# Kernel tuning notes

Hardware: AMD Instinct MI355X
Metric: run time of the kernel (lower is better)

Reference implementation:

```python
import jax, jax.numpy as jnp
import numpy as np
from jax import lax

N_NODES = 4096
M_EDGES = 16384
PDHG_ITERS = 300
POWER_ITERS = 20


def setup_inputs() -> dict:
    key = jax.random.key(0)
    kA, kb, kc = jax.random.split(key, 3)
    A = jax.random.normal(kA, (N_NODES - 2, M_EDGES), dtype=jnp.float32)
    b = jax.random.uniform(kb, (M_EDGES,), dtype=jnp.float32)  # capacities >= 0
    c = jax.random.normal(kc, (M_EDGES,), dtype=jnp.float32)
    return {"A": A, "b": b, "c": c}


def _spectral_norm(A):
    # Power iteration on A^T A; gradients stopped (step sizes are hyperparams).
    A = lax.stop_gradient(A)
    v0 = jnp.ones((A.shape[1],), A.dtype)
    v0 = v0 / jnp.linalg.norm(v0)

    def body(i, v):
        w = A.T @ (A @ v)
        return w / jnp.linalg.norm(w)

    v = lax.fori_loop(0, POWER_ITERS, body, v0)
    return jnp.sqrt(jnp.linalg.norm(A.T @ (A @ v)))


def _solve_lp(A, b, c):
    # LP:  max -c^T x  s.t.  0 <= x <= b,  A x = 0
    # <=>  min  c^T x  s.t.  x in [0, b],  A x = 0
    # Solved with PDHG (Chambolle-Pock):
    #   x <- clip(x - tau*(c + A^T y), 0, b)
    #   y <- y + sigma * A (2 x_new - x_old)
    nrm = _spectral_norm(A)
    tau = 0.9 / nrm
    sigma = 0.9 / nrm

    x0 = jnp.zeros((A.shape[1],), A.dtype)  # x = 0 is always feasible
    y0 = jnp.zeros((A.shape[0],), A.dtype)

    def step(carry, _):
        x, y = carry
        x_new = jnp.clip(x - tau * (c + A.T @ y), 0.0, b)
        y_new = y + sigma * (A @ (2.0 * x_new - x))
        return (x_new, y_new), None

    (x, y), _ = lax.scan(step, (x0, y0), None, length=PDHG_ITERS)
    return x


def reference(A, b, c):
    solution = _solve_lp(A, b, c)
    # objective == 'cost': solution.mul(-c).sum()
    return jnp.sum(solution * (-c))
```

## Files before the change

### kernel.cpp

```cpp
#include <hip/hip_runtime.h>


constexpr int N_ROWS = 4094;
constexpr int NPAD   = 4096;
constexpr int M_COLS = 16384;
constexpr int M4     = M_COLS / 4;
constexpr int PDHG_ITERS  = 300;
constexpr int POWER_ITERS = 8;
constexpr int P_CHUNKS = 64;
constexpr int ROWS_PER_CHUNK = 64;
constexpr int FJ = 32;
constexpr int FBLOCKS = M_COLS / FJ;
constexpr int AZ_J  = 64;
constexpr int AZ_CH = M_COLS / AZ_J;

typedef _Float16 half8  __attribute__((ext_vector_type(8)));
typedef _Float16 half4v __attribute__((ext_vector_type(4)));
typedef _Float16 half2v __attribute__((ext_vector_type(2)));
typedef _Float16 half_t;
typedef float f32x2 __attribute__((ext_vector_type(2)));

__device__ __forceinline__ void dec8(uint2 w, float* f) {
    f32x2 a = __builtin_amdgcn_cvt_pk_f32_fp8(w.x, false);
    f32x2 b = __builtin_amdgcn_cvt_pk_f32_fp8(w.x, true);
    f32x2 c = __builtin_amdgcn_cvt_pk_f32_fp8(w.y, false);
    f32x2 d = __builtin_amdgcn_cvt_pk_f32_fp8(w.y, true);
    f[0]=a[0]; f[1]=a[1]; f[2]=b[0]; f[3]=b[1];
    f[4]=c[0]; f[5]=c[1]; f[6]=d[0]; f[7]=d[1];
}

__global__ __launch_bounds__(256) void k_init(float* __restrict__ x,
                                              float* __restrict__ v,
                                              float* __restrict__ y,
                                              float* __restrict__ t) {
    int j = blockIdx.x * 256 + threadIdx.x;
    if (j < M_COLS) { x[j] = 0.f; v[j] = 0.0078125f; }
    if (j < NPAD) { y[j] = 0.f; t[j] = 0.f; }
}

__global__ __launch_bounds__(256) void k_transpose_both(const float* __restrict__ A,
                                                        unsigned int* __restrict__ AT8,
                                                        half_t* __restrict__ AT16) {
    __shared__ float tile[64][65];
    const int i0 = blockIdx.x * 64;
    const int j0 = blockIdx.y * 64;
    const int t = threadIdx.x;
    const float4* __restrict__ A4 = reinterpret_cast<const float4*>(A);
#pragma unroll
    for (int k = 0; k < 4; ++k) {
        int idx = k * 256 + t;
        int r = idx >> 4, c4 = idx & 15;
        int i = i0 + r;
        float4 val = (i < N_ROWS) ? A4[(size_t)i * M4 + (j0 >> 2) + c4]
                                  : make_float4(0.f, 0.f, 0.f, 0.f);
        tile[r][c4 * 4 + 0] = val.x;
        tile[r][c4 * 4 + 1] = val.y;
        tile[r][c4 * 4 + 2] = val.z;
        tile[r][c4 * 4 + 3] = val.w;
    }
    __syncthreads();
    const int it_p = i0 >> 9;
    const int sub  = (i0 >> 8) & 1;
    const int l0   = (i0 & 255) >> 2;
#pragma unroll
    for (int k = 0; k < 4; ++k) {
        int idx = k * 256 + t;
        int j = idx >> 4, lofs = idx & 15;
        float f0 = tile[lofs * 4 + 0][j] * 64.f;
        float f1 = tile[lofs * 4 + 1][j] * 64.f;
        float f2 = tile[lofs * 4 + 2][j] * 64.f;
        float f3 = tile[lofs * 4 + 3][j] * 64.f;
        int r = 0;
        r = __builtin_amdgcn_cvt_pk_fp8_f32(f0, f1, r, false);
        r = __builtin_amdgcn_cvt_pk_fp8_f32(f2, f3, r, true);
        AT8[(size_t)(j0 + j) * 1024 + it_p * 128 + (l0 + lofs) * 2 + sub] = (unsigned int)r;
    }
    half8* __restrict__ O8 = reinterpret_cast<half8*>(AT16);
#pragma unroll
    for (int k = 0; k < 2; ++k) {
        int idx = k * 256 + t;
        int j = idx >> 3, q = idx & 7;
        half8 h;
#pragma unroll
        for (int e = 0; e < 8; ++e) h[e] = (half_t)tile[q * 8 + e][j];
        O8[((size_t)(j0 + j) * NPAD + i0) / 8 + q] = h;
    }
}

__global__ __launch_bounds__(256) void k_fused8(const unsigned int* __restrict__ AT,
                                                const float* __restrict__ y,
                                                const float* __restrict__ c,
                                                const float* __restrict__ b,
                                                float* __restrict__ x,
                                                half_t* __restrict__ partial,
                                                const float* __restrict__ scalars) {
    __shared__ float ybuf[4096];
    const int tid = threadIdx.x;
    const int wv = tid >> 6, lane = tid & 63;
    {
        const float4* __restrict__ y4 = reinterpret_cast<const float4*>(y);
        float4* s4 = reinterpret_cast<float4*>(ybuf);
#pragma unroll
        for (int k = 0; k < 4; ++k) s4[k * 256 + tid] = y4[k * 256 + tid];
    }
    __syncthreads();
    const float tau = scalars[1];
    const int j0 = blockIdx.x * FJ + wv * 8;
    const uint2* __restrict__ A2 = reinterpret_cast<const uint2*>(AT);

    float xs = 0.f, cs = 0.f, bs = 0.f, xkeep = 0.f;
    if (lane < 8) {
        xs = x[j0 + lane];
        cs = c[j0 + lane];
        bs = b[j0 + lane];
    }

    float acc[64];
#pragma unroll
    for (int q = 0; q < 64; ++q) acc[q] = 0.f;

    uint2 cur[8], nxt[8];
#pragma unroll
    for (int p = 0; p < 8; ++p) cur[p] = A2[(size_t)j0 * 512 + p * 64 + lane];

    for (int q = 0; q < 8; ++q) {
        const int j = j0 + q;
        if (q + 1 < 8) {
#pragma unroll
            for (int p = 0; p < 8; ++p) nxt[p] = A2[(size_t)(j + 1) * 512 + p * 64 + lane];
        }
        float s = 0.f;
#pragma unroll
        for (int p = 0; p < 8; ++p) {
            float f[8];
            dec8(cur[p], f);
            const float4 ya = *reinterpret_cast<const float4*>(&ybuf[p * 512 + lane * 4]);
            const float4 yb = *reinterpret_cast<const float4*>(&ybuf[p * 512 + 256 + lane * 4]);
            s = fmaf(f[0], ya.x, s);
            s = fmaf(f[1], ya.y, s);
            s = fmaf(f[2], ya.z, s);
            s = fmaf(f[3], ya.w, s);
            s = fmaf(f[4], yb.x, s);
            s = fmaf(f[5], yb.y, s);
            s = fmaf(f[6], yb.z, s);
            s = fmaf(f[7], yb.w, s);
        }
#pragma unroll
        for (int o = 1; o < 64; o <<= 1) s += __shfl_xor(s, o, 64);
        s *= 0.015625f;
        float xo = __shfl(xs, q, 64);
        float cj = __shfl(cs, q, 64);
        float bj = __shfl(bs, q, 64);
        float xn = xo - tau * (cj + s);
        xn = fminf(fmaxf(xn, 0.f), bj);
        if (lane == q) xkeep = xn;
        float z = 2.f * xn - xo;
#pragma unroll
        for (int p = 0; p < 8; ++p) {
            float f[8];
            dec8(cur[p], f);
#pragma unroll
            for (int e = 0; e < 8; ++e)
                acc[p * 8 + e] = fmaf(f[e], z, acc[p * 8 + e]);
        }
#pragma unroll
        for (int p = 0; p < 8; ++p) cur[p] = nxt[p];
    }
    if (lane < 8) x[j0 + lane] = xkeep;

    __syncthreads();
    for (int w = 0; w < 4; ++w) {
        if (wv == w) {
#pragma unroll
            for (int p = 0; p < 8; ++p) {
                float4* pa = reinterpret_cast<float4*>(&ybuf[p * 512 + lane * 4]);
                float4* pb = reinterpret_cast<float4*>(&ybuf[p * 512 + 256 + lane * 4]);
                float4 va = make_float4(acc[p * 8 + 0], acc[p * 8 + 1], acc[p * 8 + 2], acc[p * 8 + 3]);
                float4 vb = make_float4(acc[p * 8 + 4], acc[p * 8 + 5], acc[p * 8 + 6], acc[p * 8 + 7]);
                if (w == 0) { *pa = va; *pb = vb; }
                else {
                    float4 oa = *pa, ob = *pb;
                    oa.x += va.x; oa.y += va.y; oa.z += va.z; oa.w += va.w;
                    ob.x += vb.x; ob.y += vb.y; ob.z += vb.z; ob.w += vb.w;
                    *pa = oa; *pb = ob;
                }
            }
        }
        __syncthreads();
    }
    half_t* __restrict__ ph = partial + (size_t)blockIdx.x * 4096;
    const float4* __restrict__ S4 = reinterpret_cast<const float4*>(ybuf);
#pragma unroll
    for (int k = 0; k < 4; ++k) {
        float4 vv = S4[k * 256 + tid];
        half4v h;
        h[0] = (half_t)vv.x; h[1] = (half_t)vv.y; h[2] = (half_t)vv.z; h[3] = (half_t)vv.w;
        *reinterpret_cast<half4v*>(&ph[k * 1024 + tid * 4]) = h;
    }
}

template <int NP>
__global__ __launch_bounds__(256) void k_merge_h(const half_t* __restrict__ partial,
                                                 float* __restrict__ y,
                                                 const float* __restrict__ scalars) {
    __shared__ float2 smf[256];
    const int tid = threadIdx.x;
    const int mb = blockIdx.x;
    const int rp = tid & 7;
    const int kk = tid >> 3;
    const half2v* __restrict__ ph2 = reinterpret_cast<const half2v*>(partial);
    float sx = 0.f, sy = 0.f;
#pragma unroll
    for (int q = 0; q < NP / 32; ++q) {
        int p = kk * (NP / 32) + q;
        half2v h = ph2[(size_t)p * 2048 + mb * 8 + rp];
        sx += (float)h[0];
        sy += (float)h[1];
    }
    smf[kk * 8 + rp] = make_float2(sx, sy);
    __syncthreads();
    if (tid < 16) {
        int pairIdx = tid >> 1, comp = tid & 1;
        float tot = 0.f;
#pragma unroll
        for (int k2 = 0; k2 < 32; ++k2) {
            float2 f2 = smf[k2 * 8 + pairIdx];
            tot += comp ? f2.y : f2.x;
        }
        y[mb * 16 + tid] += scalars[2] * tot;
    }
}

template <int NP>
__global__ __launch_bounds__(256) void k_merge0(const float* __restrict__ partial,
                                                float* __restrict__ out) {
    constexpr int PER = NP / 16;
    const int tid = threadIdx.x;
    const int r = tid & 15, k = tid >> 4;
    const int row = blockIdx.x * 16 + r;
    const float* __restrict__ p0 = partial + (size_t)k * PER * NPAD + row;
    float s = 0.f;
#pragma unroll 8
    for (int q = 0; q < PER; ++q) s += p0[(size_t)q * NPAD];
    __shared__ float sm[256];
    sm[tid] = s;
    __syncthreads();
    if (tid < 16) {
        const int orow = blockIdx.x * 16 + tid;
        float tot = 0.f;
#pragma unroll
        for (int kk = 0; kk < 16; ++kk) tot += sm[kk * 16 + tid];
        out[orow] = tot;
    }
}

__global__ __launch_bounds__(256) void k_colp8(const unsigned int* __restrict__ AT,
                                               const float* __restrict__ u,
                                               float* __restrict__ w) {
    const int wv = threadIdx.x >> 6, lane = threadIdx.x & 63;
    const int j = blockIdx.x * 4 + wv;
    const uint2* __restrict__ A2 = reinterpret_cast<const uint2*>(AT);
    const float4* __restrict__ u4 = reinterpret_cast<const float4*>(u);
    float s = 0.f;
#pragma unroll
    for (int p = 0; p < 8; ++p) {
        float f[8];
        dec8(A2[(size_t)j * 512 + p * 64 + lane], f);
        float4 ua = u4[p * 128 + lane];
        float4 ub = u4[p * 128 + 64 + lane];
        s = fmaf(f[0], ua.x, s);
        s = fmaf(f[1], ua.y, s);
        s = fmaf(f[2], ua.z, s);
        s = fmaf(f[3], ua.w, s);
        s = fmaf(f[4], ub.x, s);
        s = fmaf(f[5], ub.y, s);
        s = fmaf(f[6], ub.z, s);
        s = fmaf(f[7], ub.w, s);
    }
#pragma unroll
    for (int o = 1; o < 64; o <<= 1) s += __shfl_xor(s, o, 64);
    if (lane == 0) w[j] = s;
}

__global__ __launch_bounds__(256) void k_azp8(const unsigned int* __restrict__ AT,
                                              const float* __restrict__ zv,
                                              float* __restrict__ partial) {
    const int ch = blockIdx.y;
    const int j0 = ch * AZ_J;
    const int p = blockIdx.x * 256 + threadIdx.x;
    __shared__ float sz[AZ_J];
    if (threadIdx.x < AZ_J) sz[threadIdx.x] = zv[j0 + threadIdx.x];
    __syncthreads();
    const uint2* __restrict__ A2 = reinterpret_cast<const uint2*>(AT);
    float acc[8];
#pragma unroll
    for (int e = 0; e < 8; ++e) acc[e] = 0.f;
    for (int jj = 0; jj < AZ_J; ++jj) {
        float f[8];
        dec8(A2[(size_t)(j0 + jj) * 512 + p], f);
        float zj = sz[jj];
#pragma unroll
        for (int e = 0; e < 8; ++e) acc[e] = fmaf(f[e], zj, acc[e]);
    }
    const int ibase = (p >> 6) * 512 + (p & 63) * 4;
    float* __restrict__ P = partial + (size_t)ch * NPAD;
    *reinterpret_cast<float4*>(&P[ibase])       = make_float4(acc[0], acc[1], acc[2], acc[3]);
    *reinterpret_cast<float4*>(&P[ibase + 256]) = make_float4(acc[4], acc[5], acc[6], acc[7]);
}

template <int MODE>
__global__ __launch_bounds__(256) void k_col(const half_t* __restrict__ AT,
                                             const float* __restrict__ u,
                                             const float* __restrict__ c,
                                             const float* __restrict__ b,
                                             float* __restrict__ x,
                                             float* __restrict__ z,
                                             float* __restrict__ w,
                                             const float* __restrict__ scalars) {
    const int wv   = threadIdx.x >> 6;
    const int lane = threadIdx.x & 63;
    const int j = blockIdx.x * 4 + wv;
    const half8* __restrict__ row = reinterpret_cast<const half8*>(AT + (size_t)j * NPAD);
    const float4* __restrict__ u4 = reinterpret_cast<const float4*>(u);
    float s = 0.f;
#pragma unroll
    for (int it = 0; it < NPAD / 8 / 64; ++it) {
        int k = it * 64 + lane;
        half8 a = row[k];
        float4 ua = u4[2 * k];
        float4 ub = u4[2 * k + 1];
        s = fmaf((float)a[0], ua.x, s);
        s = fmaf((float)a[1], ua.y, s);
        s = fmaf((float)a[2], ua.z, s);
        s = fmaf((float)a[3], ua.w, s);
        s = fmaf((float)a[4], ub.x, s);
        s = fmaf((float)a[5], ub.y, s);
        s = fmaf((float)a[6], ub.z, s);
        s = fmaf((float)a[7], ub.w, s);
    }
#pragma unroll
    for (int o = 1; o < 64; o <<= 1) s += __shfl_xor(s, o, 64);
    if (lane == 0) {
        if (MODE == 0) {
            w[j] = s;
        } else {
            float tau = scalars[1];
            float xo = x[j];
            float xn = xo - tau * (c[j] + s);
            xn = fminf(fmaxf(xn, 0.f), b[j]);
            x[j] = xn;
            z[j] = 2.f * xn - xo;
        }
    }
}

__global__ __launch_bounds__(256) void k_at_partial(const float* __restrict__ A,
                                                    const float* __restrict__ u,
                                                    float* __restrict__ partial) {
    const int j4 = blockIdx.x * 256 + threadIdx.x;
    const int r0 = blockIdx.y * ROWS_PER_CHUNK;
    const int r1 = min(r0 + ROWS_PER_CHUNK, N_ROWS);
    __shared__ float su[ROWS_PER_CHUNK];
    if (threadIdx.x < (unsigned)(r1 - r0)) su[threadIdx.x] = u[r0 + threadIdx.x];
    __syncthreads();
    const float4* __restrict__ A4 = reinterpret_cast<const float4*>(A);
    float4 acc = make_float4(0.f, 0.f, 0.f, 0.f);
    for (int i = r0; i < r1; ++i) {
        const float ui = su[i - r0];
        float4 a = A4[(size_t)i * M4 + j4];
        acc.x = fmaf(a.x, ui, acc.x);
        acc.y = fmaf(a.y, ui, acc.y);
        acc.z = fmaf(a.z, ui, acc.z);
        acc.w = fmaf(a.w, ui, acc.w);
    }
    reinterpret_cast<float4*>(partial)[(size_t)blockIdx.y * M4 + j4] = acc;
}

__global__ __launch_bounds__(256) void k_reduce_w(const float* __restrict__ partial,
                                                  float* __restrict__ w) {
    int j = blockIdx.x * 256 + threadIdx.x;
    float s = 0.f;
    for (int p = 0; p < P_CHUNKS; ++p) s += partial[(size_t)p * M_COLS + j];
    w[j] = s;
}

__global__ __launch_bounds__(256) void k_x_update(const float* __restrict__ partial,
                                                  const float* __restrict__ c,
                                                  const float* __restrict__ b,
                                                  float* __restrict__ x,
                                                  float* __restrict__ z,
                                                  const float* __restrict__ scalars) {
    int j = blockIdx.x * 256 + threadIdx.x;
    const float tau = scalars[1];
    float s = 0.f;
    for (int p = 0; p < P_CHUNKS; ++p) s += partial[(size_t)p * M_COLS + j];
    float xo = x[j];
    float xn = xo - tau * (c[j] + s);
    xn = fminf(fmaxf(xn, 0.f), b[j]);
    x[j] = xn;
    z[j] = 2.f * xn - xo;
}

template <int MODE>
__global__ __launch_bounds__(256) void k_row_dot(const float* __restrict__ A,
                                                 const float* __restrict__ vec,
                                                 float* __restrict__ out,
                                                 const float* __restrict__ scalars) {
    const int i = blockIdx.x;
    const float4* __restrict__ row = reinterpret_cast<const float4*>(A + (size_t)i * M_COLS);
    const float4* __restrict__ v4  = reinterpret_cast<const float4*>(vec);
    float s = 0.f;
    for (int k = threadIdx.x; k < M4; k += 256) {
        float4 a = row[k];
        float4 v = v4[k];
        s = fmaf(a.x, v.x, s);
        s = fmaf(a.y, v.y, s);
        s = fmaf(a.z, v.z, s);
        s = fmaf(a.w, v.w, s);
    }
    for (int o = 32; o > 0; o >>= 1) s += __shfl_down(s, o, 64);
    __shared__ float sm[4];
    if ((threadIdx.x & 63) == 0) sm[threadIdx.x >> 6] = s;
    __syncthreads();
    if (threadIdx.x == 0) {
        float t = sm[0] + sm[1] + sm[2] + sm[3];
        if (MODE == 0) out[i] = t;
        else           out[i] += scalars[1] * t;
    }
}

template <int MODE>
__global__ __launch_bounds__(1024) void k_norm(const float* __restrict__ w,
                                               float* __restrict__ scalars) {
    const float4* __restrict__ w4 = reinterpret_cast<const float4*>(w);
    float s = 0.f;
    for (int k = threadIdx.x; k < M4; k += 1024) {
        float4 a = w4[k];
        s = fmaf(a.x, a.x, s);
        s = fmaf(a.y, a.y, s);
        s = fmaf(a.z, a.z, s);
        s = fmaf(a.w, a.w, s);
    }
    for (int o = 32; o > 0; o >>= 1) s += __shfl_down(s, o, 64);
    __shared__ float sm[16];
    if ((threadIdx.x & 63) == 0) sm[threadIdx.x >> 6] = s;
    __syncthreads();
    if (threadIdx.x == 0) {
        float t = 0.f;
        for (int q = 0; q < 16; ++q) t += sm[q];
        float nrm = sqrtf(t);
        if (MODE == 0) scalars[0] = nrm;
        else if (MODE == 1) {
            float tau = 57.6f / sqrtf(nrm);
            scalars[1] = tau;
            scalars[2] = tau * 0.015625f;
        } else {
            scalars[1] = 0.9f / sqrtf(nrm);
        }
    }
}

__global__ __launch_bounds__(256) void k_scale(const float* __restrict__ w,
                                               float* __restrict__ v,
                                               const float* __restrict__ scalars) {
    int j = blockIdx.x * 256 + threadIdx.x;
    v[j] = w[j] / scalars[0];
}

__global__ __launch_bounds__(1024) void k_obj(const float* __restrict__ x,
                                              const float* __restrict__ c,
                                              float* __restrict__ out) {
    float s = 0.f;
    for (int k = threadIdx.x; k < M_COLS; k += 1024) s = fmaf(x[k], -c[k], s);
    for (int o = 32; o > 0; o >>= 1) s += __shfl_down(s, o, 64);
    __shared__ float sm[16];
    if ((threadIdx.x & 63) == 0) sm[threadIdx.x >> 6] = s;
    __syncthreads();
    if (threadIdx.x == 0) {
        float t = 0.f;
        for (int q = 0; q < 16; ++q) t += sm[q];
        out[0] = t;
    }
}

extern "C" void kernel_launch(void* const* d_in, const int* in_sizes, int n_in,
                              void* d_out, int out_size, void* d_ws, size_t ws_size,
                              hipStream_t stream) {
    const float* A = (const float*)d_in[0];
    const float* b = (const float*)d_in[1];
    const float* c = (const float*)d_in[2];
    float* out = (float*)d_out;

    float* ws = (float*)d_ws;
    float* x       = ws;
    float* z       = x + M_COLS;
    float* v       = z + M_COLS;
    float* w       = v + M_COLS;
    float* y       = w + M_COLS;
    float* t       = y + NPAD;
    float* scalars = t + NPAD;
    float* partial = scalars + 16;

    size_t partial_floats = (size_t)2 * 1024 * 1024;
    size_t base = (size_t)(partial - ws) * 4 + partial_floats * 4;
    size_t a8_off = (base + 255) & ~(size_t)255;
    unsigned int* AT8 = (unsigned int*)((char*)d_ws + a8_off);
    size_t a8_bytes = (size_t)M_COLS * NPAD;
    size_t a16_off = (a8_off + a8_bytes + 255) & ~(size_t)255;
    half_t* AT16 = (half_t*)((char*)d_ws + a16_off);
    size_t a16_bytes = (size_t)M_COLS * NPAD * sizeof(half_t);
    size_t need_full = a16_off + a16_bytes;
    size_t need_fp32 = (size_t)(partial - ws) * 4 + (size_t)P_CHUNKS * M_COLS * 4;

    dim3 b256(256);
    dim3 gM(M_COLS / 256);
    dim3 gCol(M_COLS / 4);
    dim3 gFused(FBLOCKS);
    dim3 gAz(NPAD / 8 / 256, AZ_CH);
    dim3 gMerge(NPAD / 16);
    dim3 gRowA(N_ROWS);
    dim3 gTr(NPAD / 64, M_COLS / 64);

    k_init<<<gM, b256, 0, stream>>>(x, v, y, t);

    if (ws_size >= need_full) {
        k_transpose_both<<<gTr, b256, 0, stream>>>(A, AT8, AT16);

        for (int it = 0; it < POWER_ITERS; ++it) {
            k_azp8<<<gAz, b256, 0, stream>>>(AT8, v, partial);
            k_merge0<AZ_CH><<<gMerge, b256, 0, stream>>>(partial, t);
            k_colp8<<<gCol, b256, 0, stream>>>(AT8, t, w);
            k_norm<0><<<1, 1024, 0, stream>>>(w, scalars);
            k_scale<<<gM, b256, 0, stream>>>(w, v, scalars);
        }
        k_azp8<<<gAz, b256, 0, stream>>>(AT8, v, partial);
        k_merge0<AZ_CH><<<gMerge, b256, 0, stream>>>(partial, t);
        k_colp8<<<gCol, b256, 0, stream>>>(AT8, t, w);
        k_norm<1><<<1, 1024, 0, stream>>>(w, scalars);

        for (int it = 0; it < PDHG_ITERS - 1; ++it) {
            k_fused8<<<gFused, b256, 0, stream>>>(AT8, y, c, b, x,
                                                  (half_t*)partial, scalars);
            k_merge_h<FBLOCKS><<<gMerge, b256, 0, stream>>>((half_t*)partial, y, scalars);
        }
        k_col<1><<<gCol, b256, 0, stream>>>(AT16, y, c, b, x, z, w, scalars);
    } else if (ws_size >= need_fp32) {
        dim3 gAt(M4 / 256, P_CHUNKS);
        for (int it = 0; it < 20; ++it) {
            k_row_dot<0><<<gRowA, b256, 0, stream>>>(A, v, t, scalars);
            k_at_partial<<<gAt, b256, 0, stream>>>(A, t, partial);
            k_reduce_w<<<gM, b256, 0, stream>>>(partial, w);
            k_norm<0><<<1, 1024, 0, stream>>>(w, scalars);
            k_scale<<<gM, b256, 0, stream>>>(w, v, scalars);
        }
        k_row_dot<0><<<gRowA, b256, 0, stream>>>(A, v, t, scalars);
        k_at_partial<<<gAt, b256, 0, stream>>>(A, t, partial);
        k_reduce_w<<<gM, b256, 0, stream>>>(partial, w);
        k_norm<2><<<1, 1024, 0, stream>>>(w, scalars);
        for (int it = 0; it < PDHG_ITERS; ++it) {
            k_at_partial<<<gAt, b256, 0, stream>>>(A, y, partial);
            k_x_update<<<gM, b256, 0, stream>>>(partial, c, b, x, z, scalars);
            k_row_dot<1><<<gRowA, b256, 0, stream>>>(A, z, y, scalars);
        }
    }

    k_obj<<<1, 1024, 0, stream>>>(x, c, out);
}
```

Baseline: 6.216 ms.

## Use 512-thread fused PDHG blocks and fold power-iteration scaling into matvec

The fused PDHG kernel now runs 512-thread blocks covering 64 columns each, halving the number of fp16 partial slabs the merge kernel has to sum (256 instead of 512). This shrinks partial traffic and merge work per iteration, at the cost of a longer serial LDS reduction across 8 waves and lower occupancy given the 64-register accumulator per thread. Separately, the power iteration drops the k_scale launch and instead divides by the stored norm when loading the vector in the A·v kernel, with the norm initialised to 1.

```diff
diff --git a/kernel.cpp b/kernel.cpp
--- a/kernel.cpp
+++ b/kernel.cpp
@@ -9,8 +9,7 @@
 constexpr int POWER_ITERS = 8;
 constexpr int P_CHUNKS = 64;
 constexpr int ROWS_PER_CHUNK = 64;
-constexpr int FJ = 32;
-constexpr int FBLOCKS = M_COLS / FJ;
+constexpr int FBLOCKS = 256;
 constexpr int AZ_J  = 64;
 constexpr int AZ_CH = M_COLS / AZ_J;
 
@@ -32,10 +31,12 @@
 __global__ __launch_bounds__(256) void k_init(float* __restrict__ x,
                                               float* __restrict__ v,
                                               float* __restrict__ y,
-                                              float* __restrict__ t) {
+                                              float* __restrict__ t,
+                                              float* __restrict__ scalars) {
     int j = blockIdx.x * 256 + threadIdx.x;
     if (j < M_COLS) { x[j] = 0.f; v[j] = 0.0078125f; }
     if (j < NPAD) { y[j] = 0.f; t[j] = 0.f; }
+    if (j == 0) scalars[0] = 1.f;
 }
 
 __global__ __launch_bounds__(256) void k_transpose_both(const float* __restrict__ A,
@@ -87,7 +88,7 @@
     }
 }
 
-__global__ __launch_bounds__(256) void k_fused8(const unsigned int* __restrict__ AT,
+__global__ __launch_bounds__(512) void k_fused8(const unsigned int* __restrict__ AT,
                                                 const float* __restrict__ y,
                                                 const float* __restrict__ c,
                                                 const float* __restrict__ b,
@@ -101,11 +102,11 @@
         const float4* __restrict__ y4 = reinterpret_cast<const float4*>(y);
         float4* s4 = reinterpret_cast<float4*>(ybuf);
 #pragma unroll
-        for (int k = 0; k < 4; ++k) s4[k * 256 + tid] = y4[k * 256 + tid];
+        for (int k = 0; k < 2; ++k) s4[k * 512 + tid] = y4[k * 512 + tid];
     }
     __syncthreads();
     const float tau = scalars[1];
-    const int j0 = blockIdx.x * FJ + wv * 8;
+    const int j0 = blockIdx.x * 64 + wv * 8;
     const uint2* __restrict__ A2 = reinterpret_cast<const uint2*>(AT);
 
     float xs = 0.f, cs = 0.f, bs = 0.f, xkeep = 0.f;
@@ -169,7 +170,7 @@
     if (lane < 8) x[j0 + lane] = xkeep;
 
     __syncthreads();
-    for (int w = 0; w < 4; ++w) {
+    for (int w = 0; w < 8; ++w) {
         if (wv == w) {
 #pragma unroll
             for (int p = 0; p < 8; ++p) {
@@ -191,11 +192,11 @@
     half_t* __restrict__ ph = partial + (size_t)blockIdx.x * 4096;
     const float4* __restrict__ S4 = reinterpret_cast<const float4*>(ybuf);
 #pragma unroll
-    for (int k = 0; k < 4; ++k) {
-        float4 vv = S4[k * 256 + tid];
+    for (int k = 0; k < 2; ++k) {
+        float4 vv = S4[k * 512 + tid];
         half4v h;
         h[0] = (half_t)vv.x; h[1] = (half_t)vv.y; h[2] = (half_t)vv.z; h[3] = (half_t)vv.w;
-        *reinterpret_cast<half4v*>(&ph[k * 1024 + tid * 4]) = h;
+        *reinterpret_cast<half4v*>(&ph[k * 2048 + tid * 4]) = h;
     }
 }
 
@@ -282,14 +283,15 @@
     if (lane == 0) w[j] = s;
 }
 
-__global__ __launch_bounds__(256) void k_azp8(const unsigned int* __restrict__ AT,
-                                              const float* __restrict__ zv,
-                                              float* __restrict__ partial) {
+__global__ __launch_bounds__(256) void k_azp8s(const unsigned int* __restrict__ AT,
+                                               const float* __restrict__ zv,
+                                               float* __restrict__ partial,
+                                               const float* __restrict__ scalars) {
     const int ch = blockIdx.y;
     const int j0 = ch * AZ_J;
     const int p = blockIdx.x * 256 + threadIdx.x;
     __shared__ float sz[AZ_J];
-    if (threadIdx.x < AZ_J) sz[threadIdx.x] = zv[j0 + threadIdx.x];
+    if (threadIdx.x < AZ_J) sz[threadIdx.x] = zv[j0 + threadIdx.x] / scalars[0];
     __syncthreads();
     const uint2* __restrict__ A2 = reinterpret_cast<const uint2*>(AT);
     float acc[8];
@@ -513,6 +515,7 @@
     size_t need_fp32 = (size_t)(partial - ws) * 4 + (size_t)P_CHUNKS * M_COLS * 4;
 
     dim3 b256(256);
+    dim3 b512(512);
     dim3 gM(M_COLS / 256);
     dim3 gCol(M_COLS / 4);
     dim3 gFused(FBLOCKS);
@@ -521,25 +524,28 @@
     dim3 gRowA(N_ROWS);
     dim3 gTr(NPAD / 64, M_COLS / 64);
 
-    k_init<<<gM, b256, 0, stream>>>(x, v, y, t);
+    k_init<<<gM, b256, 0, stream>>>(x, v, y, t, scalars);
 
     if (ws_size >= need_full) {
         k_transpose_both<<<gTr, b256, 0, stream>>>(A, AT8, AT16);
 
-        for (int it = 0; it < POWER_ITERS; ++it) {
-            k_azp8<<<gAz, b256, 0, stream>>>(AT8, v, partial);
+        k_azp8s<<<gAz, b256, 0, stream>>>(AT8, v, partial, scalars);
+        k_merge0<AZ_CH><<<gMerge, b256, 0, stream>>>(partial, t);
+        k_colp8<<<gCol, b256, 0, stream>>>(AT8, t, w);
+        k_norm<0><<<1, 1024, 0, stream>>>(w, scalars);
+        for (int it = 1; it < POWER_ITERS; ++it) {
+            k_azp8s<<<gAz, b256, 0, stream>>>(AT8, w, partial, scalars);
             k_merge0<AZ_CH><<<gMerge, b256, 0, stream>>>(partial, t);
             k_colp8<<<gCol, b256, 0, stream>>>(AT8, t, w);
             k_norm<0><<<1, 1024, 0, stream>>>(w, scalars);
-            k_scale<<<gM, b256, 0, stream>>>(w, v, scalars);
-        }
-        k_azp8<<<gAz, b256, 0, stream>>>(AT8, v, partial);
+        }
+        k_azp8s<<<gAz, b256, 0, stream>>>(AT8, w, partial, scalars);
         k_merge0<AZ_CH><<<gMerge, b256, 0, stream>>>(partial, t);
         k_colp8<<<gCol, b256, 0, stream>>>(AT8, t, w);
         k_norm<1><<<1, 1024, 0, stream>>>(w, scalars);
 
         for (int it = 0; it < PDHG_ITERS - 1; ++it) {
-            k_fused8<<<gFused, b256, 0, stream>>>(AT8, y, c, b, x,
+            k_fused8<<<gFused, b512, 0, stream>>>(AT8, y, c, b, x,
                                                   (half_t*)partial, scalars);
             k_merge_h<FBLOCKS><<<gMerge, b256, 0, stream>>>((half_t*)partial, y, scalars);
         }
```

New measurement: 6.293 ms. Within noise of the previous version (+1.3%).
